# Kernel tuning notes

Hardware: AMD Instinct MI355X
Metric: run time of the kernel (lower is better)

## Reference

```python
import jax, jax.numpy as jnp
import numpy as np

DIM = 512
HEADS = 8
DIM_HEAD = 64
DIM_INNER = HEADS * DIM_HEAD
FRAC_GRAD = 0.5
SCALE = DIM_HEAD ** -0.5
EPS_CUMPROD = 1e-10
EPS_INV = 1e-8


def setup_inputs() -> dict:
    key = jax.random.key(0)
    ks = jax.random.split(key, 8)
    b, n = 2, 2048
    x = jax.random.normal(ks[0], (b, n, DIM), dtype=jnp.float32)
    gamma = jnp.ones((DIM,), dtype=jnp.float32)
    w_qkv = jax.random.normal(ks[1], (DIM, 3 * DIM_INNER), dtype=jnp.float32) * 0.02
    b_qkv = jnp.zeros((3 * DIM_INNER,), dtype=jnp.float32)
    # to_a: torch init is zeros weight + bias 10; use small random weight and
    # moderate bias so the decay gate is non-trivial for correctness testing
    w_a = jax.random.normal(ks[2], (DIM, DIM_INNER), dtype=jnp.float32) * 0.02
    b_a = jnp.full((DIM_INNER,), 2.0, dtype=jnp.float32)
    w_out = jax.random.normal(ks[3], (DIM_INNER, DIM), dtype=jnp.float32) * 0.02
    b_out = jnp.zeros((DIM,), dtype=jnp.float32)
    return {"x": x, "gamma": gamma, "w_qkv": w_qkv, "b_qkv": b_qkv,
            "w_a": w_a, "b_a": b_a, "w_out": w_out, "b_out": b_out}


def _rms_norm(x, gamma):
    # F.normalize(x, dim=-1) * sqrt(dim) * gamma
    nrm = jnp.linalg.norm(x, axis=-1, keepdims=True)
    return x / jnp.maximum(nrm, 1e-12) * (DIM ** 0.5) * gamma


def _safe_cumprod(t, axis):
    t = jnp.clip(t, EPS_CUMPROD, 1.0)
    return jnp.exp(jnp.cumsum(jnp.log(t), axis=axis))


def reference(x, gamma, w_qkv, b_qkv, w_a, b_a, w_out, b_out):
    b, n, _ = x.shape
    x = _rms_norm(x, gamma)

    qkv = x @ w_qkv + b_qkv  # [b, n, 3*h*d]
    qkv = qkv.reshape(b, n, 3, HEADS, DIM_HEAD).transpose(2, 0, 3, 1, 4)  # [3,b,h,n,d]
    q, k, v = qkv[0], qkv[1], qkv[2]
    q = q * SCALE

    # data-dependent relative-position decay gate
    a = (x @ w_a + b_a).reshape(b, n, HEADS, DIM_HEAD).transpose(0, 2, 1, 3)  # [b,h,n,d]
    a = a * FRAC_GRAD + jax.lax.stop_gradient(a) * (1.0 - FRAC_GRAD)
    a = jax.nn.sigmoid(a)
    a_cum = _safe_cumprod(a, axis=-2)
    a_cum_inv = 1.0 / jnp.maximum(a_cum, EPS_INV)

    q = q * a_cum
    k = k * a_cum_inv

    sim = jnp.einsum('bhid,bhjd->bhij', q, k)
    causal_mask = jnp.triu(jnp.ones((n, n), dtype=bool), k=1)
    attn = jnp.where(causal_mask, 0.0, sim)  # no softmax in decay branch

    out = jnp.einsum('bhij,bhjd->bhid', attn, v)  # [b,h,n,d]
    out = out.transpose(0, 2, 1, 3).reshape(b, n, DIM_INNER)
    return out @ w_out + b_out
```

## Files before the change

### kernel.cpp

```cpp
#include <hip/hip_runtime.h>
#include <hip/hip_cooperative_groups.h>


namespace cg = cooperative_groups;

using s8v   = __attribute__((ext_vector_type(8))) short;
using f32x4 = __attribute__((ext_vector_type(4))) float;

__device__ __forceinline__ unsigned short f2b(float f) {
  unsigned int u = __builtin_bit_cast(unsigned int, f);
  u += 0x7FFFu + ((u >> 16) & 1u);
  return (unsigned short)(u >> 16);
}
__device__ __forceinline__ float b2f(unsigned short b) {
  unsigned int u = ((unsigned int)b) << 16;
  return __builtin_bit_cast(float, u);
}
__device__ __forceinline__ f32x4 mfma16(s8v a, s8v b, f32x4 c) {
  return __builtin_amdgcn_mfma_f32_16x16x32_bf16(a, b, c, 0, 0, 0);
}
__device__ __forceinline__ void gload16(const void* g, void* l) {
  __builtin_amdgcn_global_load_lds(
      (const __attribute__((address_space(1))) void*)g,
      (__attribute__((address_space(3))) void*)l, 16, 0, 0);
}

__device__ __forceinline__ void st_prep(int u, int tid, char* arena,
    const float* __restrict__ x, const float* __restrict__ gamma,
    short* __restrict__ xnb,
    const float* __restrict__ w_qkv, const float* __restrict__ w_a,
    const float* __restrict__ w_out,
    short* __restrict__ wT, short* __restrict__ woT) {
  int lane = tid & 63, wave = tid >> 6;
  if (u < 1024) {
    int row = u * 4 + wave;
    const float4* xp = reinterpret_cast<const float4*>(x + (size_t)row * 512 + lane * 8);
    float4 v0 = xp[0], v1 = xp[1];
    float ss = v0.x*v0.x + v0.y*v0.y + v0.z*v0.z + v0.w*v0.w
             + v1.x*v1.x + v1.y*v1.y + v1.z*v1.z + v1.w*v1.w;
#pragma unroll
    for (int off = 32; off > 0; off >>= 1) ss += __shfl_xor(ss, off, 64);
    float s = 22.627416997969522f / fmaxf(sqrtf(ss), 1e-12f);
    const float* g = gamma + lane * 8;
    float vals[8] = {v0.x, v0.y, v0.z, v0.w, v1.x, v1.y, v1.z, v1.w};
    s8v o;
#pragma unroll
    for (int j = 0; j < 8; ++j) o[j] = (short)f2b(vals[j] * s * g[j]);
    *reinterpret_cast<s8v*>(xnb + (size_t)row * 512 + lane * 8) = o;
  } else {
    float (*t)[33] = reinterpret_cast<float (*)[33]>(arena);
    int id = u - 1024;
    int bx = id % 80, k0 = (id / 80) * 32;
    const float* src; short* dst; int N, n0;
    if (bx < 48)      { src = w_qkv; dst = wT;                      N = 1536; n0 = bx * 32; }
    else if (bx < 64) { src = w_a;   dst = wT + (size_t)1536 * 512; N = 512;  n0 = (bx - 48) * 32; }
    else              { src = w_out; dst = woT;                     N = 512;  n0 = (bx - 64) * 32; }
    int tx = tid & 31, ty = tid >> 5;
    __syncthreads();
#pragma unroll
    for (int i = 0; i < 4; ++i)
      t[ty + 8 * i][tx] = src[(size_t)(k0 + ty + 8 * i) * N + n0 + tx];
    __syncthreads();
#pragma unroll
    for (int i = 0; i < 4; ++i)
      dst[(size_t)(n0 + ty + 8 * i) * 512 + k0 + tx] = (short)f2b(t[tx][ty + 8 * i]);
  }
}

template <int BM, int BN, int WR, int WC>
__device__ __forceinline__ void gemm_core(const short* __restrict__ A,
                                          const short* __restrict__ Bm,
                                          char* LA, char* LB,
                                          int m0, int n0, int tid,
                                          f32x4 (&acc)[BM / WR / 16][BN / WC / 16]) {
  constexpr int WM = BM / WR, WN = BN / WC, FM = WM / 16, FN = WN / 16;
  const int lane = tid & 63, wave = tid >> 6;
  const int wr = (wave / WC) * WM, wc = (wave % WC) * WN;
#pragma unroll 1
  for (int t = 0; t < 8; ++t) {
    const int k0 = t * 64;
#pragma unroll
    for (int r = 0; r < BM / 32; ++r) {
      int o = r * 4096 + tid * 16;
      int row = o >> 7;
      int ce = (((o & 127) ^ ((row & 7) << 4)) >> 1);
      gload16(A + (size_t)(m0 + row) * 512 + k0 + ce, LA + o);
    }
#pragma unroll
    for (int r = 0; r < BN / 32; ++r) {
      int o = r * 4096 + tid * 16;
      int row = o >> 7;
      int ce = (((o & 127) ^ ((row & 7) << 4)) >> 1);
      gload16(Bm + (size_t)(n0 + row) * 512 + k0 + ce, LB + o);
    }
    __syncthreads();
#pragma unroll
    for (int kk = 0; kk < 2; ++kk) {
      s8v af[FM], bf[FN];
#pragma unroll
      for (int m = 0; m < FM; ++m) {
        int row = wr + m * 16 + (lane & 15);
        int ad = ((row << 7) + kk * 64 + ((lane >> 4) << 4)) ^ ((row & 7) << 4);
        af[m] = *reinterpret_cast<const s8v*>(LA + ad);
      }
#pragma unroll
      for (int n = 0; n < FN; ++n) {
        int row = wc + n * 16 + (lane & 15);
        int ad = ((row << 7) + kk * 64 + ((lane >> 4) << 4)) ^ ((row & 7) << 4);
        bf[n] = *reinterpret_cast<const s8v*>(LB + ad);
      }
#pragma unroll
      for (int m = 0; m < FM; ++m)
#pragma unroll
        for (int n = 0; n < FN; ++n)
          acc[m][n] = mfma16(af[m], bf[n], acc[m][n]);
    }
    if (t + 1 < 8) __syncthreads();
  }
}

__device__ __forceinline__ void st_gemm0(int vid, int tid, char* arena,
    const short* __restrict__ xnb, const short* __restrict__ wT,
    short* __restrict__ qkvb, const float* __restrict__ b_qkv,
    const float* __restrict__ b_a, float* __restrict__ araw,
    float* __restrict__ csum) {
  const int lane = tid & 63, wave = tid >> 6;
  int xcd = vid & 7, rq = vid >> 3;
  int bx = rq & 31, by = xcd * 4 + (rq >> 5);
  int m0 = by * 128, n0 = bx * 64;
  f32x4 acc[2][4] = {};
  gemm_core<128, 64, 4, 1>(xnb, wT, arena, arena + 16384, m0, n0, tid, acc);
  int wr = wave * 32;
  if (n0 < 1536) {
#pragma unroll
    for (int m = 0; m < 2; ++m)
#pragma unroll
      for (int n = 0; n < 4; ++n)
#pragma unroll
        for (int r = 0; r < 4; ++r) {
          int row = m0 + wr + m * 16 + ((lane >> 4) << 2) + r;
          int col = n0 + n * 16 + (lane & 15);
          float v = acc[m][n][r] + b_qkv[col];
          int w = col >> 9, h = (col >> 6) & 7, d = col & 63;
          int b = row >> 11, nn = row & 2047;
          qkvb[((((size_t)(w * 2 + b)) * 8 + h) * 2048 + nn) * 64 + d] = (short)f2b(v);
        }
  } else {
    __syncthreads();
    float (*WSUM)[64] = reinterpret_cast<float (*)[64]>(arena);
    float cs[4] = {};
    int b = m0 >> 11;
#pragma unroll
    for (int m = 0; m < 2; ++m)
#pragma unroll
      for (int n = 0; n < 4; ++n)
#pragma unroll
        for (int r = 0; r < 4; ++r) {
          int row = m0 + wr + m * 16 + ((lane >> 4) << 2) + r;
          int gc = n0 + n * 16 + (lane & 15) - 1536;
          int h = gc >> 6, d = gc & 63, nn = row & 2047;
          float xv = acc[m][n][r] + b_a[gc];
          araw[((size_t)(b * 8 + h) * 2048 + nn) * 64 + d] = xv;
          float a = 1.f / (1.f + expf(-xv));
          a = fminf(fmaxf(a, 1e-10f), 1.f);
          cs[n] += logf(a);
        }
#pragma unroll
    for (int n = 0; n < 4; ++n) {
      cs[n] += __shfl_xor(cs[n], 16, 64);
      cs[n] += __shfl_xor(cs[n], 32, 64);
    }
    if (lane < 16) {
#pragma unroll
      for (int n = 0; n < 4; ++n) WSUM[wave][n * 16 + lane] = cs[n];
    }
    __syncthreads();
    if (tid < 128) {
      int cl = tid >> 6, col = tid & 63;
      float s = WSUM[2 * cl][col] + WSUM[2 * cl + 1][col];
      int h = (n0 - 1536) >> 6;
      int chunkg = ((m0 & 2047) >> 6) + cl;
      csum[(((size_t)(b * 8 + h)) * 32 + chunkg) * 64 + col] = s;
    }
  }
}

__device__ __forceinline__ float csum_prefix(const float* __restrict__ csum,
                                             int bh, int chunk, int d) {
  float pre = 0.f;
#pragma unroll
  for (int c = 0; c < 32; ++c) {
    float cv = csum[((size_t)bh * 32 + c) * 64 + d];
    pre += (c < chunk) ? cv : 0.f;
  }
  return pre;
}

__device__ __forceinline__ void st_scan2(int vid, int tid, char* arena,
    const short* __restrict__ qkvb, const float* __restrict__ araw,
    const float* __restrict__ csum, short* __restrict__ q2,
    short* __restrict__ k2, short* __restrict__ vT, short* __restrict__ Sbuf) {
  int chunk = vid & 31, bh = vid >> 5;
  int lane = tid & 63, wave = tid >> 6, d = lane;
  short (*kL)[64] = reinterpret_cast<short (*)[64]>(arena);
  short (*vL)[64] = reinterpret_cast<short (*)[64]>(arena + 8192);
  char* kT  = arena + 16384;
  char* vTl = arena + 24576;
  float (*wsum)[64] = reinterpret_cast<float (*)[64]>(arena + 16384);
  float pre = csum_prefix(csum, bh, chunk, d);
  const float* ap = araw + ((size_t)bh * 2048 + chunk * 64 + wave * 16) * 64 + d;
  float la[16]; float run = 0.f;
#pragma unroll
  for (int rr = 0; rr < 16; ++rr) {
    float xv = ap[rr * 64];
    float a = 1.f / (1.f + expf(-xv));
    a = fminf(fmaxf(a, 1e-10f), 1.f);
    run += logf(a);
    la[rr] = run;
  }
  wsum[wave][d] = run;
  __syncthreads();
#pragma unroll
  for (int w = 0; w < 3; ++w) if (w < wave) pre += wsum[w][d];
  const size_t WS = (size_t)2 * 8 * 2048 * 64;
  size_t base = ((size_t)bh * 2048 + chunk * 64 + wave * 16) * 64 + d;
#pragma unroll 4
  for (int rr = 0; rr < 16; ++rr) {
    int r = wave * 16 + rr;
    float g = expf(pre + la[rr]);
    float gi = 1.f / fmaxf(g, 1e-8f);
    float qv = b2f((unsigned short)qkvb[base + rr * 64]);
    float kv = b2f((unsigned short)qkvb[base + WS + rr * 64]);
    short vb = qkvb[base + 2 * WS + rr * 64];
    q2[base + rr * 64] = (short)f2b(qv * 0.125f * g);
    unsigned short kb = f2b(kv * gi);
    k2[base + rr * 64] = (short)kb;
    kL[r][d] = (short)kb;
    vL[r][d] = vb;
  }
  __syncthreads();
  short* vTrow = vT + ((size_t)bh * 64 + d) * 2048 + chunk * 64;
#pragma unroll
  for (int gg = 0; gg < 2; ++gg) {
    int g8 = wave + gg * 4;
    s8v pk, pv;
#pragma unroll
    for (int j = 0; j < 8; ++j) { pk[j] = kL[g8 * 8 + j][d]; pv[j] = vL[g8 * 8 + j][d]; }
    *reinterpret_cast<s8v*>(vTrow + g8 * 8) = pv;
    int ad = ((d << 7) + g8 * 16) ^ ((d & 7) << 4);
    *reinterpret_cast<s8v*>(kT  + ad) = pk;
    *reinterpret_cast<s8v*>(vTl + ad) = pv;
  }
  __syncthreads();
  f32x4 acc[4] = {};
#pragma unroll
  for (int kk = 0; kk < 2; ++kk) {
    int arow = wave * 16 + (lane & 15);
    int aad = ((arow << 7) + kk * 64 + ((lane >> 4) << 4)) ^ ((arow & 7) << 4);
    s8v av = *reinterpret_cast<const s8v*>(vTl + aad);
#pragma unroll
    for (int n = 0; n < 4; ++n) {
      int brow = n * 16 + (lane & 15);
      int bad = ((brow << 7) + kk * 64 + ((lane >> 4) << 4)) ^ ((brow & 7) << 4);
      acc[n] = mfma16(av, *reinterpret_cast<const s8v*>(kT + bad), acc[n]);
    }
  }
  short* Sp = Sbuf + ((size_t)bh * 32 + chunk) * 4096;
#pragma unroll
  for (int n = 0; n < 4; ++n)
#pragma unroll
    for (int r = 0; r < 4; ++r)
      Sp[(wave * 16 + ((lane >> 4) << 2) + r) * 64 + n * 16 + (lane & 15)] = (short)f2b(acc[n][r]);
}

__device__ __forceinline__ void st_sprefix(int vid, int tid,
    const short* __restrict__ Sbuf, short* __restrict__ Spre) {
  int bh = vid >> 4;
  int e = ((vid & 15) << 8) + tid;
  size_t base = (size_t)bh * 32 * 4096 + e;
  unsigned short v[32];
#pragma unroll
  for (int c = 0; c < 32; ++c)
    v[c] = (unsigned short)Sbuf[base + (size_t)c * 4096];
  float acc = 0.f;
#pragma unroll
  for (int c = 0; c < 32; ++c) {
    Spre[base + (size_t)c * 4096] = (short)f2b(acc);
    acc += b2f(v[c]);
  }
}

__device__ __forceinline__ void st_attnk(int vid, int tid, char* arena,
    const short* __restrict__ q2, const short* __restrict__ k2,
    const short* __restrict__ vT, const short* __restrict__ Spre,
    short* __restrict__ aout) {
  int chunk = vid & 31, bh = vid >> 5;
  int lane = tid & 63, wave = tid >> 6;
  char* LQ = arena;
  char* LK = arena + 8192;
  char* LV = arena + 16384;
  char* LS = arena + 24576;
#pragma unroll
  for (int rr = 0; rr < 2; ++rr) {
    int o = rr * 4096 + tid * 16;
    int row = o >> 7;
    int ce = (((o & 127) ^ ((row & 7) << 4)) >> 1);
    gload16(q2   + ((size_t)bh * 2048 + chunk * 64 + row) * 64 + ce, LQ + o);
    gload16(k2   + ((size_t)bh * 2048 + chunk * 64 + row) * 64 + ce, LK + o);
    gload16(vT   + ((size_t)bh * 64 + row) * 2048 + chunk * 64 + ce, LV + o);
    gload16(Spre + (((size_t)bh * 32 + chunk) * 64 + row) * 64 + ce, LS + o);
  }
  __syncthreads();
  f32x4 accS[4] = {}, accO[4] = {};
#pragma unroll
  for (int kk = 0; kk < 2; ++kk) {
    int arow = wave * 16 + (lane & 15);
    int aad = ((arow << 7) + kk * 64 + ((lane >> 4) << 4)) ^ ((arow & 7) << 4);
    s8v aq = *reinterpret_cast<const s8v*>(LQ + aad);
#pragma unroll
    for (int n = 0; n < 4; ++n) {
      int brow = n * 16 + (lane & 15);
      int bad = ((brow << 7) + kk * 64 + ((lane >> 4) << 4)) ^ ((brow & 7) << 4);
      accS[n] = mfma16(aq, *reinterpret_cast<const s8v*>(LK + bad), accS[n]);
      accO[n] = mfma16(aq, *reinterpret_cast<const s8v*>(LS + bad), accO[n]);
    }
  }
  __syncthreads();
#pragma unroll
  for (int n = 0; n < 4; ++n)
#pragma unroll
    for (int r = 0; r < 4; ++r) {
      int i = wave * 16 + ((lane >> 4) << 2) + r;
      int j = n * 16 + (lane & 15);
      float v = (j <= i) ? accS[n][r] : 0.f;
      int ad = ((i << 7) + (j << 1)) ^ ((i & 7) << 4);
      *reinterpret_cast<short*>(LQ + ad) = (short)f2b(v);
    }
  __syncthreads();
#pragma unroll
  for (int kk = 0; kk < 2; ++kk) {
    int arow = wave * 16 + (lane & 15);
    int aad = ((arow << 7) + kk * 64 + ((lane >> 4) << 4)) ^ ((arow & 7) << 4);
    s8v ap = *reinterpret_cast<const s8v*>(LQ + aad);
#pragma unroll
    for (int n = 0; n < 4; ++n) {
      int brow = n * 16 + (lane & 15);
      int bad = ((brow << 7) + kk * 64 + ((lane >> 4) << 4)) ^ ((brow & 7) << 4);
      accO[n] = mfma16(ap, *reinterpret_cast<const s8v*>(LV + bad), accO[n]);
    }
  }
  int b = bh >> 3, h = bh & 7;
#pragma unroll
  for (int n = 0; n < 4; ++n)
#pragma unroll
    for (int r = 0; r < 4; ++r) {
      int i = wave * 16 + ((lane >> 4) << 2) + r;
      int col = h * 64 + n * 16 + (lane & 15);
      size_t row = (size_t)b * 2048 + chunk * 64 + i;
      aout[row * 512 + col] = (short)f2b(accO[n][r]);
    }
}

__device__ __forceinline__ void st_gemm1(int vid, int tid, char* arena,
    const short* __restrict__ aout, const short* __restrict__ woT,
    float* __restrict__ out, const float* __restrict__ b_out) {
  const int lane = tid & 63, wave = tid >> 6;
  int xcd = vid & 7, rq = vid >> 3;
  int bx = rq & 15, by = xcd * 8 + (rq >> 4);
  int m0 = by * 64, n0 = bx * 32;
  f32x4 acc[1][2] = {};
  gemm_core<64, 32, 4, 1>(aout, woT, arena, arena + 8192, m0, n0, tid, acc);
  int wr = wave * 16;
#pragma unroll
  for (int n = 0; n < 2; ++n)
#pragma unroll
    for (int r = 0; r < 4; ++r) {
      int row = m0 + wr + ((lane >> 4) << 2) + r;
      int col = n0 + n * 16 + (lane & 15);
      out[(size_t)row * 512 + col] = acc[0][n][r] + b_out[col];
    }
}

__global__ __launch_bounds__(256, 4) void mega_k(
    const float* __restrict__ x, const float* __restrict__ gamma,
    const float* __restrict__ w_qkv, const float* __restrict__ b_qkv,
    const float* __restrict__ w_a, const float* __restrict__ b_a,
    const float* __restrict__ w_out, const float* __restrict__ b_out,
    float* __restrict__ out,
    short* __restrict__ xnb, short* __restrict__ wT, short* __restrict__ woT,
    short* __restrict__ qkvb, float* __restrict__ araw, float* __restrict__ csum,
    short* __restrict__ Sbuf, short* __restrict__ aout) {
  __shared__ __align__(16) char arena[32768];
  cg::grid_group grid = cg::this_grid();
  const int bid = blockIdx.x, tid = threadIdx.x;
  const int lane = tid & 63, wave = tid >> 6;

  for (int u = bid; u < 2304; u += 1024)
    st_prep(u, tid, arena, x, gamma, xnb, w_qkv, w_a, w_out, wT, woT);
  __threadfence(); grid.sync();

  st_gemm0(bid, tid, arena, xnb, wT, qkvb, b_qkv, b_a, araw, csum);
  __threadfence(); grid.sync();

  const int unit = bid & 511;
  const int chunk = unit & 31, bh = unit >> 5;
  const int d = lane;
  char* qL  = arena;
  char* kR  = arena + 8192;
  char* kT  = arena + 16384;
  char* vTl = arena + 24576;
  f32x4 accO[4] = {};
  {
    float (*wsum)[64] = reinterpret_cast<float (*)[64]>(kR);
    float pre = csum_prefix(csum, bh, chunk, d);
    const float* ap = araw + ((size_t)bh * 2048 + chunk * 64 + wave * 16) * 64 + d;
    float la[16]; float run = 0.f;
#pragma unroll
    for (int rr = 0; rr < 16; ++rr) {
      float xv = ap[rr * 64];
      float a = 1.f / (1.f + expf(-xv));
      a = fminf(fmaxf(a, 1e-10f), 1.f);
      run += logf(a);
      la[rr] = run;
    }
    wsum[wave][d] = run;
    __syncthreads();
#pragma unroll
    for (int w = 0; w < 3; ++w) if (w < wave) pre += wsum[w][d];
    __syncthreads();
    const size_t WS = (size_t)2 * 8 * 2048 * 64;
    size_t base = ((size_t)bh * 2048 + chunk * 64 + wave * 16) * 64 + d;
#pragma unroll 4
    for (int rr = 0; rr < 16; ++rr) {
      int r = wave * 16 + rr;
      float g = expf(pre + la[rr]);
      float gi = 1.f / fmaxf(g, 1e-8f);
      float qv = b2f((unsigned short)qkvb[base + rr * 64]);
      float kv = b2f((unsigned short)qkvb[base + WS + rr * 64]);
      short vb = qkvb[base + 2 * WS + rr * 64];
      unsigned short qb = f2b(qv * 0.125f * g);
      unsigned short kb = f2b(kv * gi);
      int adr = ((r << 7) + (d << 1)) ^ ((r & 7) << 4);
      *reinterpret_cast<short*>(qL + adr) = (short)qb;
      *reinterpret_cast<short*>(kR + adr) = (short)kb;
      int adt = ((d << 7) + (r << 1)) ^ ((d & 7) << 4);
      *reinterpret_cast<short*>(kT  + adt) = (short)kb;
      *reinterpret_cast<short*>(vTl + adt) = vb;
    }
    __syncthreads();
    f32x4 sacc[4] = {};
#pragma unroll
    for (int kk = 0; kk < 2; ++kk) {
      int arow = wave * 16 + (lane & 15);
      int aad = ((arow << 7) + kk * 64 + ((lane >> 4) << 4)) ^ ((arow & 7) << 4);
      s8v av = *reinterpret_cast<const s8v*>(vTl + aad);
#pragma unroll
      for (int n = 0; n < 4; ++n) {
        int brow = n * 16 + (lane & 15);
        int bad = ((brow << 7) + kk * 64 + ((lane >> 4) << 4)) ^ ((brow & 7) << 4);
        sacc[n] = mfma16(av, *reinterpret_cast<const s8v*>(kT + bad), sacc[n]);
      }
    }
    short* Sp = Sbuf + ((size_t)bh * 32 + chunk) * 4096;
#pragma unroll
    for (int n = 0; n < 4; ++n)
#pragma unroll
      for (int r = 0; r < 4; ++r)
        Sp[(wave * 16 + ((lane >> 4) << 2) + r) * 64 + n * 16 + (lane & 15)] = (short)f2b(sacc[n][r]);
    f32x4 accS[4] = {};
#pragma unroll
    for (int kk = 0; kk < 2; ++kk) {
      int arow = wave * 16 + (lane & 15);
      int aad = ((arow << 7) + kk * 64 + ((lane >> 4) << 4)) ^ ((arow & 7) << 4);
      s8v aq = *reinterpret_cast<const s8v*>(qL + aad);
#pragma unroll
      for (int n = 0; n < 4; ++n) {
        int brow = n * 16 + (lane & 15);
        int bad = ((brow << 7) + kk * 64 + ((lane >> 4) << 4)) ^ ((brow & 7) << 4);
        accS[n] = mfma16(aq, *reinterpret_cast<const s8v*>(kR + bad), accS[n]);
      }
    }
    __syncthreads();
#pragma unroll
    for (int n = 0; n < 4; ++n)
#pragma unroll
      for (int r = 0; r < 4; ++r) {
        int i = wave * 16 + ((lane >> 4) << 2) + r;
        int j = n * 16 + (lane & 15);
        float v = (j <= i) ? accS[n][r] : 0.f;
        int ad = ((i << 7) + (j << 1)) ^ ((i & 7) << 4);
        *reinterpret_cast<short*>(kT + ad) = (short)f2b(v);
      }
    __syncthreads();
#pragma unroll
    for (int kk = 0; kk < 2; ++kk) {
      int arow = wave * 16 + (lane & 15);
      int aad = ((arow << 7) + kk * 64 + ((lane >> 4) << 4)) ^ ((arow & 7) << 4);
      s8v ap = *reinterpret_cast<const s8v*>(kT + aad);
#pragma unroll
      for (int n = 0; n < 4; ++n) {
        int brow = n * 16 + (lane & 15);
        int bad = ((brow << 7) + kk * 64 + ((lane >> 4) << 4)) ^ ((brow & 7) << 4);
        accO[n] = mfma16(ap, *reinterpret_cast<const s8v*>(vTl + bad), accO[n]);
      }
    }
  }
  __threadfence(); grid.sync();

  {
    char* LS = kR;
    int srow = tid >> 2, scol0 = (tid & 3) * 16;
    const short* Sb = Sbuf + (size_t)bh * 32 * 4096 + srow * 64 + scol0;
    float acc0[8] = {}, acc1[8] = {};
#pragma unroll
    for (int c = 0; c < 32; ++c) {
      if (c < chunk) {
        s8v v0 = *reinterpret_cast<const s8v*>(Sb + (size_t)c * 4096);
        s8v v1 = *reinterpret_cast<const s8v*>(Sb + (size_t)c * 4096 + 8);
#pragma unroll
        for (int j = 0; j < 8; ++j) {
          acc0[j] += b2f((unsigned short)v0[j]);
          acc1[j] += b2f((unsigned short)v1[j]);
        }
      }
    }
    s8v o0, o1;
#pragma unroll
    for (int j = 0; j < 8; ++j) {
      o0[j] = (short)f2b(acc0[j]);
      o1[j] = (short)f2b(acc1[j]);
    }
    int byte0 = (srow << 7) + (scol0 << 1);
    int sw = (srow & 7) << 4;
    *reinterpret_cast<s8v*>(LS + ((byte0)      ^ sw)) = o0;
    *reinterpret_cast<s8v*>(LS + ((byte0 + 16) ^ sw)) = o1;
    __syncthreads();
#pragma unroll
    for (int kk = 0; kk < 2; ++kk) {
      int arow = wave * 16 + (lane & 15);
      int aad = ((arow << 7) + kk * 64 + ((lane >> 4) << 4)) ^ ((arow & 7) << 4);
      s8v aq = *reinterpret_cast<const s8v*>(qL + aad);
#pragma unroll
      for (int n = 0; n < 4; ++n) {
        int brow = n * 16 + (lane & 15);
        int bad = ((brow << 7) + kk * 64 + ((lane >> 4) << 4)) ^ ((brow & 7) << 4);
        accO[n] = mfma16(aq, *reinterpret_cast<const s8v*>(LS + bad), accO[n]);
      }
    }
    int b = bh >> 3, h = bh & 7;
#pragma unroll
    for (int n = 0; n < 4; ++n)
#pragma unroll
      for (int r = 0; r < 4; ++r) {
        int i = wave * 16 + ((lane >> 4) << 2) + r;
        int col = h * 64 + n * 16 + (lane & 15);
        size_t row = (size_t)b * 2048 + chunk * 64 + i;
        aout[row * 512 + col] = (short)f2b(accO[n][r]);
      }
  }
  __threadfence(); grid.sync();

  st_gemm1(bid, tid, arena, aout, woT, out, b_out);
}

__global__ __launch_bounds__(256) void prep_k(const float* x, const float* gamma,
    short* xnb, const float* w_qkv, const float* w_a, const float* w_out,
    short* wT, short* woT) {
  __shared__ __align__(16) char arena[4224];
  st_prep(blockIdx.x, threadIdx.x, arena, x, gamma, xnb, w_qkv, w_a, w_out, wT, woT);
}
__global__ __launch_bounds__(256) void gemm0_k(const short* xnb, const short* wT,
    short* qkvb, const float* b_qkv, const float* b_a, float* araw, float* csum) {
  __shared__ __align__(16) char arena[24576];
  st_gemm0(blockIdx.x, threadIdx.x, arena, xnb, wT, qkvb, b_qkv, b_a, araw, csum);
}
__global__ __launch_bounds__(256) void scan2_k(const short* qkvb, const float* araw,
    const float* csum, short* q2, short* k2, short* vT, short* Sbuf) {
  __shared__ __align__(16) char arena[32768];
  st_scan2(blockIdx.x, threadIdx.x, arena, qkvb, araw, csum, q2, k2, vT, Sbuf);
}
__global__ __launch_bounds__(256) void sprefix_k(const short* Sbuf, short* Spre) {
  st_sprefix(blockIdx.x, threadIdx.x, Sbuf, Spre);
}
__global__ __launch_bounds__(256) void attnk_k(const short* q2, const short* k2,
    const short* vT, const short* Spre, short* aout) {
  __shared__ __align__(16) char arena[32768];
  st_attnk(blockIdx.x, threadIdx.x, arena, q2, k2, vT, Spre, aout);
}
__global__ __launch_bounds__(256) void gemm1_k(const short* aout, const short* woT,
    float* out, const float* b_out) {
  __shared__ __align__(16) char arena[12288];
  st_gemm1(blockIdx.x, threadIdx.x, arena, aout, woT, out, b_out);
}

extern "C" void kernel_launch(void* const* d_in, const int* in_sizes, int n_in,
                              void* d_out, int out_size, void* d_ws, size_t ws_size,
                              hipStream_t stream) {
  const float* x     = (const float*)d_in[0];
  const float* gamma = (const float*)d_in[1];
  const float* w_qkv = (const float*)d_in[2];
  const float* b_qkv = (const float*)d_in[3];
  const float* w_a   = (const float*)d_in[4];
  const float* b_a   = (const float*)d_in[5];
  const float* w_out = (const float*)d_in[6];
  const float* b_out = (const float*)d_in[7];
  float* out = (float*)d_out;
  char* ws = (char*)d_ws;

  const size_t MB = 1u << 20;
  short* xnb  = (short*)(ws);
  short* wT   = (short*)(ws + 4  * MB);
  short* woT  = (short*)(ws + 6  * MB);
  short* qkvb = (short*)(ws + 7  * MB);
  float* araw = (float*)(ws + 19 * MB);
  float* csum = (float*)(ws + 27 * MB);
  short* Sbuf = (short*)(ws + 28 * MB);
  short* aout = (short*)(ws + 32 * MB);
  short* Spre = (short*)(ws + 36 * MB);
  short* q2   = (short*)(ws + 40 * MB);
  short* k2   = (short*)(ws + 44 * MB);
  short* vT   = (short*)(ws + 48 * MB);

  int dev = 0; (void)hipGetDevice(&dev);
  int coop = 0;
  (void)hipDeviceGetAttribute(&coop, hipDeviceAttributeCooperativeLaunch, dev);
  int nb = 0;
  (void)hipOccupancyMaxActiveBlocksPerMultiprocessor(&nb, mega_k, 256, 0);

  hipError_t err = hipErrorUnknown;
  if (coop && nb >= 4) {
    void* args[] = {&x, &gamma, &w_qkv, &b_qkv, &w_a, &b_a, &w_out, &b_out,
                    &out, &xnb, &wT, &woT, &qkvb, &araw, &csum,
                    &Sbuf, &aout};
    err = hipLaunchCooperativeKernel((void*)mega_k, dim3(1024), dim3(256), args, 0, stream);
  }
  if (err != hipSuccess) {
    prep_k   <<<2304, 256, 0, stream>>>(x, gamma, xnb, w_qkv, w_a, w_out, wT, woT);
    gemm0_k  <<<1024, 256, 0, stream>>>(xnb, wT, qkvb, b_qkv, b_a, araw, csum);
    scan2_k  <<<512,  256, 0, stream>>>(qkvb, araw, csum, q2, k2, vT, Sbuf);
    sprefix_k<<<256,  256, 0, stream>>>(Sbuf, Spre);
    attnk_k  <<<512,  256, 0, stream>>>(q2, k2, vT, Spre, aout);
    gemm1_k  <<<1024, 256, 0, stream>>>(aout, woT, out, b_out);
  }
}
```

Before: 59.68 us.

## Double-buffer LDS in GEMM core and retile gemm0 to 64x64 with 2x2 waves

```diff
diff --git a/kernel.cpp b/kernel.cpp
--- a/kernel.cpp
+++ b/kernel.cpp
@@ -68,17 +68,18 @@
 }
 
 template <int BM, int BN, int WR, int WC>
-__device__ __forceinline__ void gemm_core(const short* __restrict__ A,
-                                          const short* __restrict__ Bm,
-                                          char* LA, char* LB,
-                                          int m0, int n0, int tid,
-                                          f32x4 (&acc)[BM / WR / 16][BN / WC / 16]) {
+__device__ __forceinline__ void gemm_core_db(const short* __restrict__ A,
+                                             const short* __restrict__ Bm,
+                                             char* LA0, char* LA1,
+                                             char* LB0, char* LB1,
+                                             int m0, int n0, int tid,
+                                             f32x4 (&acc)[BM / WR / 16][BN / WC / 16]) {
   constexpr int WM = BM / WR, WN = BN / WC, FM = WM / 16, FN = WN / 16;
   const int lane = tid & 63, wave = tid >> 6;
   const int wr = (wave / WC) * WM, wc = (wave % WC) * WN;
-#pragma unroll 1
-  for (int t = 0; t < 8; ++t) {
-    const int k0 = t * 64;
+
+  auto stage = [&](int t, char* LA, char* LB) {
+    int k0 = t * 64;
 #pragma unroll
     for (int r = 0; r < BM / 32; ++r) {
       int o = r * 4096 + tid * 16;
@@ -93,7 +94,18 @@
       int ce = (((o & 127) ^ ((row & 7) << 4)) >> 1);
       gload16(Bm + (size_t)(n0 + row) * 512 + k0 + ce, LB + o);
     }
-    __syncthreads();
+  };
+
+  stage(0, LA0, LB0);
+  __syncthreads();
+  int cur = 0;
+#pragma unroll 1
+  for (int t = 0; t < 8; ++t) {
+    char* sLA = cur ? LA0 : LA1;
+    char* sLB = cur ? LB0 : LB1;
+    char* cLA = cur ? LA1 : LA0;
+    char* cLB = cur ? LB1 : LB0;
+    if (t + 1 < 8) stage(t + 1, sLA, sLB);
 #pragma unroll
     for (int kk = 0; kk < 2; ++kk) {
       s8v af[FM], bf[FN];
@@ -101,13 +113,13 @@
       for (int m = 0; m < FM; ++m) {
         int row = wr + m * 16 + (lane & 15);
         int ad = ((row << 7) + kk * 64 + ((lane >> 4) << 4)) ^ ((row & 7) << 4);
-        af[m] = *reinterpret_cast<const s8v*>(LA + ad);
+        af[m] = *reinterpret_cast<const s8v*>(cLA + ad);
       }
 #pragma unroll
       for (int n = 0; n < FN; ++n) {
         int row = wc + n * 16 + (lane & 15);
         int ad = ((row << 7) + kk * 64 + ((lane >> 4) << 4)) ^ ((row & 7) << 4);
-        bf[n] = *reinterpret_cast<const s8v*>(LB + ad);
+        bf[n] = *reinterpret_cast<const s8v*>(cLB + ad);
       }
 #pragma unroll
       for (int m = 0; m < FM; ++m)
@@ -115,7 +127,8 @@
         for (int n = 0; n < FN; ++n)
           acc[m][n] = mfma16(af[m], bf[n], acc[m][n]);
     }
-    if (t + 1 < 8) __syncthreads();
+    __syncthreads();
+    cur ^= 1;
   }
 }
 
@@ -126,61 +139,68 @@
     float* __restrict__ csum) {
   const int lane = tid & 63, wave = tid >> 6;
   int xcd = vid & 7, rq = vid >> 3;
-  int bx = rq & 31, by = xcd * 4 + (rq >> 5);
-  int m0 = by * 128, n0 = bx * 64;
-  f32x4 acc[2][4] = {};
-  gemm_core<128, 64, 4, 1>(xnb, wT, arena, arena + 16384, m0, n0, tid, acc);
-  int wr = wave * 32;
-  if (n0 < 1536) {
-#pragma unroll
-    for (int m = 0; m < 2; ++m)
-#pragma unroll
-      for (int n = 0; n < 4; ++n)
-#pragma unroll
-        for (int r = 0; r < 4; ++r) {
-          int row = m0 + wr + m * 16 + ((lane >> 4) << 2) + r;
-          int col = n0 + n * 16 + (lane & 15);
-          float v = acc[m][n][r] + b_qkv[col];
-          int w = col >> 9, h = (col >> 6) & 7, d = col & 63;
-          int b = row >> 11, nn = row & 2047;
-          qkvb[((((size_t)(w * 2 + b)) * 8 + h) * 2048 + nn) * 64 + d] = (short)f2b(v);
+  int npair = rq & 15, my = xcd * 8 + (rq >> 4);
+  int m0 = my * 64;
+#pragma unroll 1
+  for (int tt = 0; tt < 2; ++tt) {
+    int n0 = npair * 128 + tt * 64;
+    __syncthreads();
+    f32x4 acc[2][2] = {};
+    gemm_core_db<64, 64, 2, 2>(xnb, wT, arena, arena + 8192,
+                               arena + 16384, arena + 24576, m0, n0, tid, acc);
+    int wr = (wave >> 1) * 32, wc = (wave & 1) * 32;
+    if (n0 < 1536) {
+#pragma unroll
+      for (int m = 0; m < 2; ++m)
+#pragma unroll
+        for (int n = 0; n < 2; ++n)
+#pragma unroll
+          for (int r = 0; r < 4; ++r) {
+            int row = m0 + wr + m * 16 + ((lane >> 4) << 2) + r;
+            int col = n0 + wc + n * 16 + (lane & 15);
+            float v = acc[m][n][r] + b_qkv[col];
+            int w = col >> 9, h = (col >> 6) & 7, d = col & 63;
+            int b = row >> 11, nn = row & 2047;
+            qkvb[((((size_t)(w * 2 + b)) * 8 + h) * 2048 + nn) * 64 + d] = (short)f2b(v);
+          }
+    } else {
+      float cs[2] = {};
+      int b = m0 >> 11;
+#pragma unroll
+      for (int m = 0; m < 2; ++m)
+#pragma unroll
+        for (int n = 0; n < 2; ++n)
+#pragma unroll
+          for (int r = 0; r < 4; ++r) {
+            int row = m0 + wr + m * 16 + ((lane >> 4) << 2) + r;
+            int gc = n0 + wc + n * 16 + (lane & 15) - 1536;
+            int h = gc >> 6, d = gc & 63, nn = row & 2047;
+            float xv = acc[m][n][r] + b_a[gc];
+            araw[((size_t)(b * 8 + h) * 2048 + nn) * 64 + d] = xv;
+            float a = 1.f / (1.f + expf(-xv));
+            a = fminf(fmaxf(a, 1e-10f), 1.f);
+            cs[n] += logf(a);
+          }
+#pragma unroll
+      for (int n = 0; n < 2; ++n) {
+        cs[n] += __shfl_xor(cs[n], 16, 64);
+        cs[n] += __shfl_xor(cs[n], 32, 64);
+      }
+      float (*WSUM)[64] = reinterpret_cast<float (*)[64]>(arena);
+      if (lane < 16) {
+#pragma unroll
+        for (int n2 = 0; n2 < 4; ++n2) {
+          bool mine = (n2 >> 1) == (wave & 1);
+          WSUM[wave][n2 * 16 + lane] = mine ? cs[n2 & 1] : 0.f;
         }
-  } else {
-    __syncthreads();
-    float (*WSUM)[64] = reinterpret_cast<float (*)[64]>(arena);
-    float cs[4] = {};
-    int b = m0 >> 11;
-#pragma unroll
-    for (int m = 0; m < 2; ++m)
-#pragma unroll
-      for (int n = 0; n < 4; ++n)
-#pragma unroll
-        for (int r = 0; r < 4; ++r) {
-          int row = m0 + wr + m * 16 + ((lane >> 4) << 2) + r;
-          int gc = n0 + n * 16 + (lane & 15) - 1536;
-          int h = gc >> 6, d = gc & 63, nn = row & 2047;
-          float xv = acc[m][n][r] + b_a[gc];
-          araw[((size_t)(b * 8 + h) * 2048 + nn) * 64 + d] = xv;
-          float a = 1.f / (1.f + expf(-xv));
-          a = fminf(fmaxf(a, 1e-10f), 1.f);
-          cs[n] += logf(a);
-        }
-#pragma unroll
-    for (int n = 0; n < 4; ++n) {
-      cs[n] += __shfl_xor(cs[n], 16, 64);
-      cs[n] += __shfl_xor(cs[n], 32, 64);
-    }
-    if (lane < 16) {
-#pragma unroll
-      for (int n = 0; n < 4; ++n) WSUM[wave][n * 16 + lane] = cs[n];
-    }
-    __syncthreads();
-    if (tid < 128) {
-      int cl = tid >> 6, col = tid & 63;
-      float s = WSUM[2 * cl][col] + WSUM[2 * cl + 1][col];
-      int h = (n0 - 1536) >> 6;
-      int chunkg = ((m0 & 2047) >> 6) + cl;
-      csum[(((size_t)(b * 8 + h)) * 32 + chunkg) * 64 + col] = s;
+      }
+      __syncthreads();
+      if (tid < 64) {
+        float s = (WSUM[0][tid] + WSUM[1][tid]) + (WSUM[2][tid] + WSUM[3][tid]);
+        int h = (n0 - 1536) >> 6;
+        int chunkg = (m0 & 2047) >> 6;
+        csum[(((size_t)(b * 8 + h)) * 32 + chunkg) * 64 + tid] = s;
+      }
     }
   }
 }
@@ -369,7 +389,8 @@
   int bx = rq & 15, by = xcd * 8 + (rq >> 4);
   int m0 = by * 64, n0 = bx * 32;
   f32x4 acc[1][2] = {};
-  gemm_core<64, 32, 4, 1>(aout, woT, arena, arena + 8192, m0, n0, tid, acc);
+  gemm_core_db<64, 32, 4, 1>(aout, woT, arena, arena + 8192,
+                             arena + 16384, arena + 20480, m0, n0, tid, acc);
   int wr = wave * 16;
 #pragma unroll
   for (int n = 0; n < 2; ++n)
@@ -571,7 +592,7 @@
 }
 __global__ __launch_bounds__(256) void gemm0_k(const short* xnb, const short* wT,
     short* qkvb, const float* b_qkv, const float* b_a, float* araw, float* csum) {
-  __shared__ __align__(16) char arena[24576];
+  __shared__ __align__(16) char arena[32768];
   st_gemm0(blockIdx.x, threadIdx.x, arena, xnb, wT, qkvb, b_qkv, b_a, araw, csum);
 }
 __global__ __launch_bounds__(256) void scan2_k(const short* qkvb, const float* araw,
@@ -589,7 +610,7 @@
 }
 __global__ __launch_bounds__(256) void gemm1_k(const short* aout, const short* woT,
     float* out, const float* b_out) {
-  __shared__ __align__(16) char arena[12288];
+  __shared__ __align__(16) char arena[24576];
   st_gemm1(blockIdx.x, threadIdx.x, arena, aout, woT, out, b_out);
 }
 
```

Result: slower. 63.67 us (+6.7%).

## Fuse QKV/gate GEMM into per-chunk attention block, drop qkv/araw round trip

Applied to the files above, without the earlier changes.

```diff
diff --git a/kernel.cpp b/kernel.cpp
--- a/kernel.cpp
+++ b/kernel.cpp
@@ -119,7 +119,18 @@
   }
 }
 
-__device__ __forceinline__ void st_gemm0(int vid, int tid, char* arena,
+__device__ __forceinline__ float csum_prefix(const float* __restrict__ csum,
+                                             int bh, int chunk, int d) {
+  float pre = 0.f;
+#pragma unroll
+  for (int c = 0; c < 32; ++c) {
+    float cv = csum[((size_t)bh * 32 + c) * 64 + d];
+    pre += (c < chunk) ? cv : 0.f;
+  }
+  return pre;
+}
+
+__device__ __forceinline__ void st_gemm0_fb(int vid, int tid, char* arena,
     const short* __restrict__ xnb, const short* __restrict__ wT,
     short* __restrict__ qkvb, const float* __restrict__ b_qkv,
     const float* __restrict__ b_a, float* __restrict__ araw,
@@ -183,17 +194,6 @@
       csum[(((size_t)(b * 8 + h)) * 32 + chunkg) * 64 + col] = s;
     }
   }
-}
-
-__device__ __forceinline__ float csum_prefix(const float* __restrict__ csum,
-                                             int bh, int chunk, int d) {
-  float pre = 0.f;
-#pragma unroll
-  for (int c = 0; c < 32; ++c) {
-    float cv = csum[((size_t)bh * 32 + c) * 64 + d];
-    pre += (c < chunk) ? cv : 0.f;
-  }
-  return pre;
 }
 
 __device__ __forceinline__ void st_scan2(int vid, int tid, char* arena,
@@ -361,7 +361,7 @@
     }
 }
 
-__device__ __forceinline__ void st_gemm1(int vid, int tid, char* arena,
+__device__ __forceinline__ void st_gemm1_fb(int vid, int tid, char* arena,
     const short* __restrict__ aout, const short* __restrict__ woT,
     float* __restrict__ out, const float* __restrict__ b_out) {
   const int lane = tid & 63, wave = tid >> 6;
@@ -381,71 +381,171 @@
     }
 }
 
-__global__ __launch_bounds__(256, 4) void mega_k(
+__global__ __launch_bounds__(256, 2) void mega_k(
     const float* __restrict__ x, const float* __restrict__ gamma,
     const float* __restrict__ w_qkv, const float* __restrict__ b_qkv,
     const float* __restrict__ w_a, const float* __restrict__ b_a,
     const float* __restrict__ w_out, const float* __restrict__ b_out,
     float* __restrict__ out,
     short* __restrict__ xnb, short* __restrict__ wT, short* __restrict__ woT,
-    short* __restrict__ qkvb, float* __restrict__ araw, float* __restrict__ csum,
-    short* __restrict__ Sbuf, short* __restrict__ aout) {
-  __shared__ __align__(16) char arena[32768];
+    float* __restrict__ csum, short* __restrict__ Sbuf, short* __restrict__ aout) {
+  __shared__ __align__(16) char arena[57600];
   cg::grid_group grid = cg::this_grid();
   const int bid = blockIdx.x, tid = threadIdx.x;
   const int lane = tid & 63, wave = tid >> 6;
 
-  for (int u = bid; u < 2304; u += 1024)
+  for (int u = bid; u < 2304; u += 512)
     st_prep(u, tid, arena, x, gamma, xnb, w_qkv, w_a, w_out, wT, woT);
   __threadfence(); grid.sync();
 
-  st_gemm0(bid, tid, arena, xnb, wT, qkvb, b_qkv, b_a, araw, csum);
-  __threadfence(); grid.sync();
-
-  const int unit = bid & 511;
-  const int chunk = unit & 31, bh = unit >> 5;
-  const int d = lane;
+  const int xcd = bid & 7, idx = bid >> 3;
+  const int bh = xcd * 2 + (idx >> 5);
+  const int chunk = idx & 31;
+  const int b = bh >> 3, h = bh & 7;
+
   char* qL  = arena;
   char* kR  = arena + 8192;
   char* kT  = arena + 16384;
   char* vTl = arena + 24576;
-  f32x4 accO[4] = {};
+  float* laBuf = reinterpret_cast<float*>(arena + 40960);
+  float (*wsumA)[64] = reinterpret_cast<float (*)[64]>(arena + 32768);
+  float* preArr = reinterpret_cast<float*>(arena + 32768);
+
+  f32x4 acc[4][4] = {};
   {
-    float (*wsum)[64] = reinterpret_cast<float (*)[64]>(kR);
-    float pre = csum_prefix(csum, bh, chunk, d);
-    const float* ap = araw + ((size_t)bh * 2048 + chunk * 64 + wave * 16) * 64 + d;
-    float la[16]; float run = 0.f;
+    const int m0g = b * 2048 + chunk * 64;
+    char* LBp = arena + 8192 + wave * 8192;
+#pragma unroll 1
+    for (int t = 0; t < 8; ++t) {
+      int k0 = t * 64;
+#pragma unroll
+      for (int r = 0; r < 2; ++r) {
+        int o = r * 4096 + tid * 16;
+        int row = o >> 7;
+        int ce = (((o & 127) ^ ((row & 7) << 4)) >> 1);
+        gload16(xnb + (size_t)(m0g + row) * 512 + k0 + ce, arena + o);
+      }
+#pragma unroll
+      for (int p = 0; p < 4; ++p)
+#pragma unroll
+        for (int r = 0; r < 2; ++r) {
+          int o = r * 4096 + tid * 16;
+          int row = o >> 7;
+          int ce = (((o & 127) ^ ((row & 7) << 4)) >> 1);
+          gload16(wT + (size_t)(p * 512 + h * 64 + row) * 512 + k0 + ce,
+                  arena + 8192 + p * 8192 + o);
+        }
+      __syncthreads();
+#pragma unroll
+      for (int kk = 0; kk < 2; ++kk) {
+        s8v af[4], bf[4];
+#pragma unroll
+        for (int m = 0; m < 4; ++m) {
+          int row = m * 16 + (lane & 15);
+          int ad = ((row << 7) + kk * 64 + ((lane >> 4) << 4)) ^ ((row & 7) << 4);
+          af[m] = *reinterpret_cast<const s8v*>(arena + ad);
+        }
+#pragma unroll
+        for (int n = 0; n < 4; ++n) {
+          int row = n * 16 + (lane & 15);
+          int ad = ((row << 7) + kk * 64 + ((lane >> 4) << 4)) ^ ((row & 7) << 4);
+          bf[n] = *reinterpret_cast<const s8v*>(LBp + ad);
+        }
+#pragma unroll
+        for (int m = 0; m < 4; ++m)
+#pragma unroll
+          for (int n = 0; n < 4; ++n)
+            acc[m][n] = mfma16(af[m], bf[n], acc[m][n]);
+      }
+      __syncthreads();
+    }
+  }
+  if (wave == 2) {
+#pragma unroll
+    for (int m = 0; m < 4; ++m)
+#pragma unroll
+      for (int n = 0; n < 4; ++n)
+#pragma unroll
+        for (int r = 0; r < 4; ++r) {
+          int row = m * 16 + ((lane >> 4) << 2) + r;
+          int col = n * 16 + (lane & 15);
+          float vv = acc[m][n][r] + b_qkv[1024 + h * 64 + col];
+          int adt = ((col << 7) + (row << 1)) ^ ((col & 7) << 4);
+          *reinterpret_cast<short*>(vTl + adt) = (short)f2b(vv);
+        }
+  } else if (wave == 3) {
+#pragma unroll
+    for (int m = 0; m < 4; ++m)
+#pragma unroll
+      for (int n = 0; n < 4; ++n)
+#pragma unroll
+        for (int r = 0; r < 4; ++r) {
+          int row = m * 16 + ((lane >> 4) << 2) + r;
+          int col = n * 16 + (lane & 15);
+          laBuf[row * 65 + col] = acc[m][n][r] + b_a[h * 64 + col];
+        }
+  }
+  __syncthreads();
+  {
+    float la_loc[16]; float run = 0.f;
 #pragma unroll
     for (int rr = 0; rr < 16; ++rr) {
-      float xv = ap[rr * 64];
+      float xv = laBuf[(wave * 16 + rr) * 65 + lane];
       float a = 1.f / (1.f + expf(-xv));
       a = fminf(fmaxf(a, 1e-10f), 1.f);
       run += logf(a);
-      la[rr] = run;
-    }
-    wsum[wave][d] = run;
-    __syncthreads();
-#pragma unroll
-    for (int w = 0; w < 3; ++w) if (w < wave) pre += wsum[w][d];
-    __syncthreads();
-    const size_t WS = (size_t)2 * 8 * 2048 * 64;
-    size_t base = ((size_t)bh * 2048 + chunk * 64 + wave * 16) * 64 + d;
-#pragma unroll 4
-    for (int rr = 0; rr < 16; ++rr) {
-      int r = wave * 16 + rr;
-      float g = expf(pre + la[rr]);
-      float gi = 1.f / fmaxf(g, 1e-8f);
-      float qv = b2f((unsigned short)qkvb[base + rr * 64]);
-      float kv = b2f((unsigned short)qkvb[base + WS + rr * 64]);
-      short vb = qkvb[base + 2 * WS + rr * 64];
-      unsigned short qb = f2b(qv * 0.125f * g);
-      unsigned short kb = f2b(kv * gi);
-      int adr = ((r << 7) + (d << 1)) ^ ((r & 7) << 4);
-      *reinterpret_cast<short*>(qL + adr) = (short)qb;
-      *reinterpret_cast<short*>(kR + adr) = (short)kb;
-      int adt = ((d << 7) + (r << 1)) ^ ((d & 7) << 4);
-      *reinterpret_cast<short*>(kT  + adt) = (short)kb;
-      *reinterpret_cast<short*>(vTl + adt) = vb;
+      la_loc[rr] = run;
+    }
+    wsumA[wave][lane] = run;
+    __syncthreads();
+    float prew = 0.f;
+#pragma unroll
+    for (int w = 0; w < 3; ++w) if (w < wave) prew += wsumA[w][lane];
+#pragma unroll
+    for (int rr = 0; rr < 16; ++rr)
+      laBuf[(wave * 16 + rr) * 65 + lane] = prew + la_loc[rr];
+    if (tid < 64) {
+      float s = ((wsumA[0][tid] + wsumA[1][tid]) + wsumA[2][tid]) + wsumA[3][tid];
+      csum[(((size_t)bh) * 32 + chunk) * 64 + tid] = s;
+    }
+  }
+  __threadfence(); grid.sync();
+
+  f32x4 accO[4] = {};
+  {
+    if (tid < 64) preArr[tid] = csum_prefix(csum, bh, chunk, tid);
+    __syncthreads();
+    if (wave == 0) {
+#pragma unroll
+      for (int m = 0; m < 4; ++m)
+#pragma unroll
+        for (int n = 0; n < 4; ++n)
+#pragma unroll
+          for (int r = 0; r < 4; ++r) {
+            int row = m * 16 + ((lane >> 4) << 2) + r;
+            int col = n * 16 + (lane & 15);
+            float g = expf(preArr[col] + laBuf[row * 65 + col]);
+            float qv = (acc[m][n][r] + b_qkv[h * 64 + col]) * 0.125f * g;
+            int adr = ((row << 7) + (col << 1)) ^ ((row & 7) << 4);
+            *reinterpret_cast<short*>(qL + adr) = (short)f2b(qv);
+          }
+    } else if (wave == 1) {
+#pragma unroll
+      for (int m = 0; m < 4; ++m)
+#pragma unroll
+        for (int n = 0; n < 4; ++n)
+#pragma unroll
+          for (int r = 0; r < 4; ++r) {
+            int row = m * 16 + ((lane >> 4) << 2) + r;
+            int col = n * 16 + (lane & 15);
+            float gi = 1.f / fmaxf(expf(preArr[col] + laBuf[row * 65 + col]), 1e-8f);
+            float kv = (acc[m][n][r] + b_qkv[512 + h * 64 + col]) * gi;
+            unsigned short kb = f2b(kv);
+            int adr = ((row << 7) + (col << 1)) ^ ((row & 7) << 4);
+            int adt = ((col << 7) + (row << 1)) ^ ((col & 7) << 4);
+            *reinterpret_cast<short*>(kR + adr) = (short)kb;
+            *reinterpret_cast<short*>(kT + adt) = (short)kb;
+          }
     }
     __syncthreads();
     f32x4 sacc[4] = {};
@@ -547,7 +647,6 @@
         accO[n] = mfma16(aq, *reinterpret_cast<const s8v*>(LS + bad), accO[n]);
       }
     }
-    int b = bh >> 3, h = bh & 7;
 #pragma unroll
     for (int n = 0; n < 4; ++n)
 #pragma unroll
@@ -560,7 +659,24 @@
   }
   __threadfence(); grid.sync();
 
-  st_gemm1(bid, tid, arena, aout, woT, out, b_out);
+  {
+    int xcd6 = bid & 7, rq = bid >> 3;
+    int bx = rq & 7, by = xcd6 * 8 + (rq >> 3);
+    int m0 = by * 64, n0 = bx * 64;
+    f32x4 a6[2][2] = {};
+    gemm_core<64, 64, 2, 2>(aout, woT, arena, arena + 8192, m0, n0, tid, a6);
+    int wr = (wave >> 1) * 32, wc = (wave & 1) * 32;
+#pragma unroll
+    for (int m = 0; m < 2; ++m)
+#pragma unroll
+      for (int n = 0; n < 2; ++n)
+#pragma unroll
+        for (int r = 0; r < 4; ++r) {
+          int row = m0 + wr + m * 16 + ((lane >> 4) << 2) + r;
+          int col = n0 + wc + n * 16 + (lane & 15);
+          out[(size_t)row * 512 + col] = a6[m][n][r] + b_out[col];
+        }
+  }
 }
 
 __global__ __launch_bounds__(256) void prep_k(const float* x, const float* gamma,
@@ -572,7 +688,7 @@
 __global__ __launch_bounds__(256) void gemm0_k(const short* xnb, const short* wT,
     short* qkvb, const float* b_qkv, const float* b_a, float* araw, float* csum) {
   __shared__ __align__(16) char arena[24576];
-  st_gemm0(blockIdx.x, threadIdx.x, arena, xnb, wT, qkvb, b_qkv, b_a, araw, csum);
+  st_gemm0_fb(blockIdx.x, threadIdx.x, arena, xnb, wT, qkvb, b_qkv, b_a, araw, csum);
 }
 __global__ __launch_bounds__(256) void scan2_k(const short* qkvb, const float* araw,
     const float* csum, short* q2, short* k2, short* vT, short* Sbuf) {
@@ -590,7 +706,7 @@
 __global__ __launch_bounds__(256) void gemm1_k(const short* aout, const short* woT,
     float* out, const float* b_out) {
   __shared__ __align__(16) char arena[12288];
-  st_gemm1(blockIdx.x, threadIdx.x, arena, aout, woT, out, b_out);
+  st_gemm1_fb(blockIdx.x, threadIdx.x, arena, aout, woT, out, b_out);
 }
 
 extern "C" void kernel_launch(void* const* d_in, const int* in_sizes, int n_in,
@@ -611,11 +727,11 @@
   short* xnb  = (short*)(ws);
   short* wT   = (short*)(ws + 4  * MB);
   short* woT  = (short*)(ws + 6  * MB);
-  short* qkvb = (short*)(ws + 7  * MB);
-  float* araw = (float*)(ws + 19 * MB);
-  float* csum = (float*)(ws + 27 * MB);
-  short* Sbuf = (short*)(ws + 28 * MB);
-  short* aout = (short*)(ws + 32 * MB);
+  float* csum = (float*)(ws + 7  * MB);
+  short* Sbuf = (short*)(ws + 8  * MB);
+  short* aout = (short*)(ws + 12 * MB);
+  short* qkvb = (short*)(ws + 16 * MB);
+  float* araw = (float*)(ws + 28 * MB);
   short* Spre = (short*)(ws + 36 * MB);
   short* q2   = (short*)(ws + 40 * MB);
   short* k2   = (short*)(ws + 44 * MB);
@@ -628,11 +744,10 @@
   (void)hipOccupancyMaxActiveBlocksPerMultiprocessor(&nb, mega_k, 256, 0);
 
   hipError_t err = hipErrorUnknown;
-  if (coop && nb >= 4) {
+  if (coop && nb >= 2) {
     void* args[] = {&x, &gamma, &w_qkv, &b_qkv, &w_a, &b_a, &w_out, &b_out,
-                    &out, &xnb, &wT, &woT, &qkvb, &araw, &csum,
-                    &Sbuf, &aout};
-    err = hipLaunchCooperativeKernel((void*)mega_k, dim3(1024), dim3(256), args, 0, stream);
+                    &out, &xnb, &wT, &woT, &csum, &Sbuf, &aout};
+    err = hipLaunchCooperativeKernel((void*)mega_k, dim3(512), dim3(256), args, 0, stream);
   }
   if (err != hipSuccess) {
     prep_k   <<<2304, 256, 0, stream>>>(x, gamma, xnb, w_qkv, w_a, w_out, wT, woT);
```

After: 59.24 us. No clear change (-0.7%).
